# Kernel optimization log

Measured on AMD Instinct MI355X. Metric: run time of the kernel, lower is better.

## Reference

```python
import jax, jax.numpy as jnp
import numpy as np

B, T, F, U = 8192, 21, 3, 512


def setup_inputs() -> dict:
    key = jax.random.key(0)
    ks = jax.random.split(key, 10)
    s = 0.05  # weight scale
    return {
        "x": jax.random.normal(ks[0], (B, T, F), jnp.float32),
        "learn_type_all": jax.random.randint(ks[1], (T, B), 0, 2).astype(jnp.int32),
        "kernel": jax.random.normal(ks[2], (F, 4 * U), jnp.float32) * s,
        "recurrent_kernel": jax.random.normal(ks[3], (U, 4 * U), jnp.float32) * s,
        "bias": jnp.zeros((4 * U,), jnp.float32),
        "w_rnn": jax.random.normal(ks[4], (U, U), jnp.float32) * s,
        "u_rnn": jax.random.normal(ks[5], (U, U), jnp.float32) * s,
        "b_rnn": jnp.zeros((U,), jnp.float32),
        "w_fc": jax.random.normal(ks[6], (U, 32), jnp.float32) * s,
        "b_fc": jnp.zeros((32,), jnp.float32),
        "w_out": jax.random.normal(ks[7], (32, 1), jnp.float32) * s,
        "b_out": jnp.zeros((1,), jnp.float32),
    }


def _forward(x, learn_type_all, kernel, recurrent_kernel, bias,
             w_rnn, u_rnn, b_rnn, w_fc, b_fc, w_out, b_out):
    # Per-timestep, per-batch-row learn mask; if a timestep has no learned row,
    # the original forces row 0 to learn.
    mask = learn_type_all == 1                      # [T, B]
    any_learn = jnp.any(mask, axis=1)               # [T]
    mask = mask.at[:, 0].set(mask[:, 0] | ~any_learn)

    # For each row i, the output gate o comes from the most recent learned row
    # j <= i (forward fill); leading unlearned rows take the FIRST learned row's o.
    pos = jnp.where(mask, jnp.arange(B)[None, :], -1)      # [T, B]
    last_idx = jax.lax.cummax(pos, axis=1)                 # [T, B]
    first = jnp.argmax(mask, axis=1)                       # [T]
    o_idx = jnp.where(last_idx < 0, first[:, None], last_idx)  # [T, B]

    xs = jnp.moveaxis(x, 1, 0)  # [T, B, F]

    def lstm_cell(carry, inp):
        h, c = carry
        x_t, m_t, idx_t = inp
        # fused gate compute (implementation=2 path of the original)
        z = x_t @ kernel + h @ recurrent_kernel + bias     # [B, 4U]
        zi, zf, zg, zo = jnp.split(z, 4, axis=1)
        i_g = jax.nn.sigmoid(zi)
        f_g = jax.nn.sigmoid(zf)
        g_g = jnp.tanh(zg)
        o_comp = jax.nn.sigmoid(zo)
        # learned rows update carry; unlearned rows keep c_tm1
        c_new = jnp.where(m_t[:, None], f_g * c + i_g * g_g, c)
        o = o_comp[idx_t]                                  # gather prev-learned o
        h_new = o * jnp.tanh(c_new)
        return (h_new, c_new), h_new

    init = (jnp.zeros((B, U), x.dtype), jnp.zeros((B, U), x.dtype))
    (_, _), hs = jax.lax.scan(lstm_cell, init, (xs, mask, o_idx))  # hs: [T, B, U]

    # SimpleRNN over the LSTM output sequence (dropout inactive at inference)
    def srnn_cell(h, x_t):
        h_new = jnp.tanh(x_t @ w_rnn + h @ u_rnn + b_rnn)
        return h_new, None

    h_last, _ = jax.lax.scan(srnn_cell, jnp.zeros((B, U), x.dtype), hs)

    out = (h_last @ w_fc + b_fc) @ w_out + b_out           # [B, 1]
    return out


def reference(x, learn_type_all, kernel, recurrent_kernel, bias,
              w_rnn, u_rnn, b_rnn, w_fc, b_fc, w_out, b_out):
    return _forward(x, learn_type_all, kernel, recurrent_kernel, bias,
                    w_rnn, u_rnn, b_rnn, w_fc, b_fc, w_out, b_out)
```

## Files before the change

### kernel.cpp

```cpp
#include <hip/hip_runtime.h>
#include <stdint.h>

#define B_ 8192
#define T_ 21
#define F_ 3
#define U_ 512

typedef _Float16 f16x8 __attribute__((ext_vector_type(8)));
typedef float f32x4 __attribute__((ext_vector_type(4)));

__device__ __forceinline__ float fsigmoid(float x) { return 1.0f / (1.0f + __expf(-x)); }
__device__ __forceinline__ float ftanh_(float x) {
  float t = __expf(-2.0f * fabsf(x));
  float r = (1.0f - t) / (1.0f + t);
  return x < 0.0f ? -r : r;
}

__device__ __forceinline__ void gl_lds16(const void* g, void* l) {
  __builtin_amdgcn_global_load_lds((__attribute__((address_space(1))) void*)g,
                                   (__attribute__((address_space(3))) void*)l, 16, 0, 0);
}

__global__ void prep_weights(const float* __restrict__ Wr, const float* __restrict__ wrnn,
                             const float* __restrict__ urnn, const float* __restrict__ kern,
                             const float* __restrict__ bias,
                             _Float16* __restrict__ WrT, _Float16* __restrict__ W2T,
                             float* __restrict__ Kp, float* __restrict__ bp) {
  size_t i = (size_t)blockIdx.x * 256 + threadIdx.x;
  if (i < (size_t)2048 * 512) {
    int p = (int)(i >> 9), k = (int)(i & 511);
    int orig = ((p >> 4) & 3) * 512 + ((p >> 6) << 4) + (p & 15);
    WrT[i] = (_Float16)Wr[(size_t)k * 2048 + orig];
  }
  if (i < (size_t)512 * 1024) {
    int n = (int)(i >> 10), k = (int)(i & 1023);
    float v = (k < 512) ? wrnn[(size_t)k * 512 + n] : urnn[(size_t)(k - 512) * 512 + n];
    W2T[i] = (_Float16)v;
  }
  if (i < 2048) {
    int p = (int)i;
    int orig = ((p >> 4) & 3) * 512 + ((p >> 6) << 4) + (p & 15);
    Kp[p] = kern[orig];
    Kp[2048 + p] = kern[2048 + orig];
    Kp[4096 + p] = kern[4096 + orig];
    bp[p] = bias[orig];
  }
}

__global__ void prep_wv(const float* __restrict__ wfc, const float* __restrict__ bfc,
                        const float* __restrict__ wout, const float* __restrict__ bout,
                        float* __restrict__ wv) {
  int u = blockIdx.x * 256 + threadIdx.x;
  if (u < 512) {
    float s = 0.0f;
    for (int k = 0; k < 32; ++k) s += wfc[u * 32 + k] * wout[k];
    wv[u] = s;
  }
  if (u == 0) {
    float s = 0.0f;
    for (int k = 0; k < 32; ++k) s += bfc[k] * wout[k];
    wv[512] = s + bout[0];
  }
}

__global__ void prep_mask(const int* __restrict__ lt, int* __restrict__ orow,
                          int* __restrict__ idxL, int* __restrict__ Mpad) {
  const int t = blockIdx.x;
  const int tid = threadIdx.x;
  __shared__ int sh[1024];
  __shared__ int s_any, s_first;
  if (tid == 0) { s_any = 0; s_first = 0x7fffffff; }
  __syncthreads();
  const int base = tid * 8;
  const int* row = lt + (size_t)t * B_ + base;
  int bits = 0;
#pragma unroll
  for (int j = 0; j < 8; ++j) bits |= (row[j] == 1) << j;
  if (bits) atomicOr(&s_any, 1);
  __syncthreads();
  if (tid == 0 && !s_any) bits |= 1;
  if (bits) atomicMin(&s_first, base + __ffs(bits) - 1);
  int lmax = -1;
#pragma unroll
  for (int j = 0; j < 8; ++j)
    if ((bits >> j) & 1) lmax = base + j;
  sh[tid] = lmax;
  __syncthreads();
  for (int off = 1; off < 1024; off <<= 1) {
    int v = (tid >= off) ? sh[tid - off] : -1;
    __syncthreads();
    if (v > sh[tid]) sh[tid] = v;
    __syncthreads();
  }
  const int prefix = (tid > 0) ? sh[tid - 1] : -1;
  __syncthreads();
  const int cnt = __popc(bits);
  sh[tid] = cnt;
  __syncthreads();
  for (int off = 1; off < 1024; off <<= 1) {
    int v = (tid >= off) ? sh[tid - off] : 0;
    __syncthreads();
    sh[tid] += v;
    __syncthreads();
  }
  const int excl = sh[tid] - cnt;
  const int total = sh[1023];
  const int first = s_first;
  int run = prefix, pos = excl;
  int* orp = orow + (size_t)t * B_ + base;
  int* ixp = idxL + (size_t)t * B_;
#pragma unroll
  for (int j = 0; j < 8; ++j) {
    if ((bits >> j) & 1) { ixp[pos++] = base + j; run = base + j; }
    orp[j] = (run < 0) ? first : run;
  }
  const int padded = (total + 127) & ~127;
  if (tid < padded - total) ixp[total + tid] = -1;
  if (tid == 0) Mpad[t] = padded;
}

template <int MODE>
__device__ __forceinline__ void gemm_body(
    _Float16 (*__restrict__ Ab)[4096], _Float16 (*__restrict__ Bb)[4096],
    const _Float16* __restrict__ A0, const _Float16* __restrict__ A1,
    const _Float16* __restrict__ Wt, const float* __restrict__ x,
    const float* __restrict__ Kp, const float* __restrict__ bp,
    float* __restrict__ cbuf, _Float16* __restrict__ og,
    const float* __restrict__ brnn, _Float16* __restrict__ rout,
    const int* __restrict__ idxL, int mBase, int nBase, int t) {
  constexpr int K = (MODE == 0) ? 512 : 1024;
  constexpr int NT = K / 32;
  const int tid = threadIdx.x;
  const int w = tid >> 6, l = tid & 63;
  const int wm = w >> 1, wn = w & 1;
  const int lr = l >> 2;
  const int lk = (l & 3) * 8;
  const int ch0 = w * 2, ch1 = w * 2 + 1;

  int ra0, ra1;
  if constexpr (MODE == 0) {
    int i0 = idxL[mBase + ch0 * 16 + lr];
    int i1 = idxL[mBase + ch1 * 16 + lr];
    ra0 = i0 < 0 ? 0 : i0;
    ra1 = i1 < 0 ? 0 : i1;
  } else {
    ra0 = mBase + ch0 * 16 + lr;
    ra1 = mBase + ch1 * 16 + lr;
  }

  auto STAGE = [&](int bb, int kt) {
    const int k0 = kt * 32;
    const _Float16* As = A0;
    int koff = k0;
    if constexpr (MODE == 1) {
      if (k0 >= 512) { As = A1; koff = k0 - 512; }
    }
    gl_lds16(As + (size_t)ra0 * 512 + koff + lk, (char*)Ab[bb] + ch0 * 1024);
    gl_lds16(As + (size_t)ra1 * 512 + koff + lk, (char*)Ab[bb] + ch1 * 1024);
    gl_lds16(Wt + (size_t)(nBase + ch0 * 16 + lr) * K + k0 + lk, (char*)Bb[bb] + ch0 * 1024);
    gl_lds16(Wt + (size_t)(nBase + ch1 * 16 + lr) * K + k0 + lk, (char*)Bb[bb] + ch1 * 1024);
  };

  f32x4 acc[4][4] = {};
  STAGE(0, 0);
  const int frow = l & 15;
  const int fkb = (l >> 4) * 8;
  for (int kt = 0; kt < NT; ++kt) {
    __syncthreads();
    if (kt + 1 < NT) STAGE((kt + 1) & 1, kt + 1);
    const int bb = kt & 1;
    f16x8 af[4], bf[4];
#pragma unroll
    for (int m = 0; m < 4; ++m)
      af[m] = *(const f16x8*)&Ab[bb][(wm * 64 + m * 16 + frow) * 32 + fkb];
#pragma unroll
    for (int n = 0; n < 4; ++n)
      bf[n] = *(const f16x8*)&Bb[bb][(wn * 64 + n * 16 + frow) * 32 + fkb];
#pragma unroll
    for (int m = 0; m < 4; ++m)
#pragma unroll
      for (int n = 0; n < 4; ++n)
        acc[m][n] = __builtin_amdgcn_mfma_f32_16x16x32_f16(af[m], bf[n], acc[m][n], 0, 0, 0);
  }

  const int c_ = l & 15, rg = l >> 4;
  const int pB = nBase + wn * 64;
  if constexpr (MODE == 0) {
    const int u = (pB >> 6) * 16 + c_;
    float kf[4][3], bb4[4];
#pragma unroll
    for (int n = 0; n < 4; ++n) {
      int p = pB + n * 16 + c_;
      kf[n][0] = Kp[p]; kf[n][1] = Kp[2048 + p]; kf[n][2] = Kp[4096 + p];
      bb4[n] = bp[p];
    }
#pragma unroll
    for (int m = 0; m < 4; ++m) {
#pragma unroll
      for (int r = 0; r < 4; ++r) {
        int bi = idxL[mBase + wm * 64 + m * 16 + rg * 4 + r];
        if (bi < 0) continue;
        const float* xp = x + (size_t)bi * (T_ * F_) + t * F_;
        float x0 = xp[0], x1 = xp[1], x2 = xp[2];
        float zi = acc[m][0][r] + x0 * kf[0][0] + x1 * kf[0][1] + x2 * kf[0][2] + bb4[0];
        float zf = acc[m][1][r] + x0 * kf[1][0] + x1 * kf[1][1] + x2 * kf[1][2] + bb4[1];
        float zg = acc[m][2][r] + x0 * kf[2][0] + x1 * kf[2][1] + x2 * kf[2][2] + bb4[2];
        float zo = acc[m][3][r] + x0 * kf[3][0] + x1 * kf[3][1] + x2 * kf[3][2] + bb4[3];
        float ig = fsigmoid(zi), fg = fsigmoid(zf);
        float gg = ftanh_(zg), ogv = fsigmoid(zo);
        size_t ci = (size_t)bi * 512 + u;
        float cold = cbuf[ci];
        cbuf[ci] = fg * cold + ig * gg;
        og[ci] = (_Float16)ogv;
      }
    }
  } else {
#pragma unroll
    for (int m = 0; m < 4; ++m)
#pragma unroll
      for (int n = 0; n < 4; ++n) {
        int uu = pB + n * 16 + c_;
        float bn = brnn[uu];
#pragma unroll
        for (int r = 0; r < 4; ++r) {
          int b = mBase + wm * 64 + m * 16 + rg * 4 + r;
          rout[(size_t)b * 512 + uu] = (_Float16)ftanh_(acc[m][n][r] + bn);
        }
      }
  }
}

__global__ __launch_bounds__(256, 2) void fused_step(
    const _Float16* __restrict__ h, const _Float16* __restrict__ rin,
    _Float16* __restrict__ rot, const _Float16* __restrict__ WrT,
    const _Float16* __restrict__ W2T, const float* __restrict__ x,
    const float* __restrict__ Kp, const float* __restrict__ bp,
    float* __restrict__ cbuf, _Float16* __restrict__ og,
    const float* __restrict__ brnn, const int* __restrict__ idxL,
    const int* __restrict__ MpadP, int t) {
  __shared__ __align__(16) _Float16 Ab[2][4096];
  __shared__ __align__(16) _Float16 Bb[2][4096];
  if (blockIdx.y < 16) {
    if ((int)blockIdx.x * 128 >= *MpadP) return;
    gemm_body<0>(Ab, Bb, h, nullptr, WrT, x, Kp, bp, cbuf, og, nullptr, nullptr,
                 idxL, blockIdx.x * 128, blockIdx.y * 128, t);
  } else {
    gemm_body<1>(Ab, Bb, h, rin, W2T, nullptr, nullptr, nullptr, nullptr, nullptr,
                 brnn, rot, nullptr, blockIdx.x * 128, ((int)blockIdx.y - 16) * 128, t);
  }
}

__global__ __launch_bounds__(256, 2) void rnn_tail(
    const _Float16* __restrict__ h, const _Float16* __restrict__ rin,
    const _Float16* __restrict__ W2T, const float* __restrict__ brnn,
    _Float16* __restrict__ rot) {
  __shared__ __align__(16) _Float16 Ab[2][4096];
  __shared__ __align__(16) _Float16 Bb[2][4096];
  gemm_body<1>(Ab, Bb, h, rin, W2T, nullptr, nullptr, nullptr, nullptr, nullptr,
               brnn, rot, nullptr, blockIdx.x * 128, blockIdx.y * 128, 0);
}

__global__ void gather_h(const _Float16* __restrict__ og, const float* __restrict__ cbuf,
                         const int* __restrict__ orow, _Float16* __restrict__ h) {
  int g = blockIdx.x * 256 + threadIdx.x;
  int b = g >> 6, u0 = (g & 63) << 3;
  int src = orow[b];
  f16x8 ov = *(const f16x8*)(og + (size_t)src * 512 + u0);
  const float4* cp = (const float4*)(cbuf + (size_t)b * 512 + u0);
  float4 c0 = cp[0], c1 = cp[1];
  float cc[8] = {c0.x, c0.y, c0.z, c0.w, c1.x, c1.y, c1.z, c1.w};
  f16x8 hv;
#pragma unroll
  for (int j = 0; j < 8; ++j) hv[j] = (_Float16)((float)ov[j] * ftanh_(cc[j]));
  *(f16x8*)(h + (size_t)b * 512 + u0) = hv;
}

__global__ void final_fc(const _Float16* __restrict__ r, const float* __restrict__ wv,
                         float* __restrict__ out) {
  int gw = (blockIdx.x * 256 + threadIdx.x) >> 6;
  int l = threadIdx.x & 63;
  const _Float16* rr = r + (size_t)gw * 512;
  f16x8 rv = *(const f16x8*)(rr + l * 8);
  const float4* wp = (const float4*)(wv + l * 8);
  float4 w0 = wp[0], w1 = wp[1];
  float wf[8] = {w0.x, w0.y, w0.z, w0.w, w1.x, w1.y, w1.z, w1.w};
  float s = 0.0f;
#pragma unroll
  for (int j = 0; j < 8; ++j) s += (float)rv[j] * wf[j];
  for (int o = 32; o; o >>= 1) s += __shfl_down(s, o);
  if (l == 0) out[gw] = s + wv[512];
}

extern "C" void kernel_launch(void* const* d_in, const int* in_sizes, int n_in,
                              void* d_out, int out_size, void* d_ws, size_t ws_size,
                              hipStream_t stream) {
  const float* x    = (const float*)d_in[0];
  const int*   lt   = (const int*)d_in[1];
  const float* kern = (const float*)d_in[2];
  const float* Wr   = (const float*)d_in[3];
  const float* bias = (const float*)d_in[4];
  const float* wrnn = (const float*)d_in[5];
  const float* urnn = (const float*)d_in[6];
  const float* brnn = (const float*)d_in[7];
  const float* wfc  = (const float*)d_in[8];
  const float* bfc  = (const float*)d_in[9];
  const float* wout = (const float*)d_in[10];
  const float* bout = (const float*)d_in[11];

  char* ws = (char*)d_ws;
  size_t off = 0;
  auto alloc = [&](size_t bytes) {
    void* p = ws + off;
    off = (off + bytes + 255) & ~(size_t)255;
    return p;
  };
  int*      orow = (int*)alloc((size_t)T_ * B_ * 4);
  int*      idxL = (int*)alloc((size_t)T_ * B_ * 4);
  int*      Mpad = (int*)alloc(T_ * 4);
  float*    cbuf = (float*)alloc((size_t)B_ * U_ * 4);
  _Float16* h    = (_Float16*)alloc((size_t)B_ * U_ * 2);
  _Float16* r0   = (_Float16*)alloc((size_t)B_ * U_ * 2);
  _Float16* r1   = (_Float16*)alloc((size_t)B_ * U_ * 2);
  _Float16* og   = (_Float16*)alloc((size_t)B_ * U_ * 2);
  _Float16* WrT  = (_Float16*)alloc((size_t)2048 * 512 * 2);
  _Float16* W2T  = (_Float16*)alloc((size_t)512 * 1024 * 2);
  float*    Kp   = (float*)alloc(3 * 2048 * 4);
  float*    bp   = (float*)alloc(2048 * 4);
  float*    wv   = (float*)alloc(516 * 4);

  hipMemsetAsync(cbuf, 0, (size_t)B_ * U_ * 4, stream);
  hipMemsetAsync(h, 0, (size_t)B_ * U_ * 2, stream);
  hipMemsetAsync(r0, 0, (size_t)B_ * U_ * 2, stream);

  prep_weights<<<4096, 256, 0, stream>>>(Wr, wrnn, urnn, kern, bias, WrT, W2T, Kp, bp);
  prep_wv<<<2, 256, 0, stream>>>(wfc, bfc, wout, bout, wv);
  prep_mask<<<T_, 1024, 0, stream>>>(lt, orow, idxL, Mpad);

  _Float16* rin = r0;
  _Float16* rot = r1;
  fused_step<<<dim3(64, 16), 256, 0, stream>>>(h, nullptr, nullptr, WrT, W2T, x, Kp, bp,
                                               cbuf, og, brnn, idxL, Mpad, 0);
  gather_h<<<2048, 256, 0, stream>>>(og, cbuf, orow, h);
  for (int t = 1; t < T_; ++t) {
    fused_step<<<dim3(64, 20), 256, 0, stream>>>(h, rin, rot, WrT, W2T, x, Kp, bp,
                                                 cbuf, og, brnn,
                                                 idxL + (size_t)t * B_, Mpad + t, t);
    _Float16* tmp = rin; rin = rot; rot = tmp;
    gather_h<<<2048, 256, 0, stream>>>(og, cbuf, orow + (size_t)t * B_, h);
  }
  rnn_tail<<<dim3(64, 4), 256, 0, stream>>>(h, rin, W2T, brnn, rot);
  final_fc<<<2048, 256, 0, stream>>>(rot, wv, (float*)d_out);
}
```

Before: 1.025 ms.

## Triple-buffer GEMM LDS pipeline and compute learned-row h in epilogue

The GEMM main loop moves from a double-buffered LDS stage with one barrier per step to a three-stage ring. It prefetches two K-tiles ahead and uses explicit vmcnt waits and raw barriers, with launch bounds raised to 3 blocks per CU. The LSTM epilogue now writes h directly for learned rows into a double-buffered h array. prep_mask builds an index list of unlearned rows so gather_h only processes those rows. This aims to hide global-load latency and cut gather work, at the cost of more LDS per block, an extra h buffer, and fragile hand-tuned waitcnt counts.

```diff
diff --git a/kernel.cpp b/kernel.cpp
--- a/kernel.cpp
+++ b/kernel.cpp
@@ -64,7 +64,8 @@
 }
 
 __global__ void prep_mask(const int* __restrict__ lt, int* __restrict__ orow,
-                          int* __restrict__ idxL, int* __restrict__ Mpad) {
+                          int* __restrict__ idxL, int* __restrict__ idxU,
+                          int* __restrict__ Mpad) {
   const int t = blockIdx.x;
   const int tid = threadIdx.x;
   __shared__ int sh[1024];
@@ -106,16 +107,20 @@
   const int excl = sh[tid] - cnt;
   const int total = sh[1023];
   const int first = s_first;
-  int run = prefix, pos = excl;
+  int run = prefix, posL = excl, posU = base - excl;
   int* orp = orow + (size_t)t * B_ + base;
-  int* ixp = idxL + (size_t)t * B_;
+  int* ixL = idxL + (size_t)t * B_;
+  int* ixU = idxU + (size_t)t * B_;
 #pragma unroll
   for (int j = 0; j < 8; ++j) {
-    if ((bits >> j) & 1) { ixp[pos++] = base + j; run = base + j; }
+    if ((bits >> j) & 1) { ixL[posL++] = base + j; run = base + j; }
+    else                 { ixU[posU++] = base + j; }
     orp[j] = (run < 0) ? first : run;
   }
   const int padded = (total + 127) & ~127;
-  if (tid < padded - total) ixp[total + tid] = -1;
+  if (tid < padded - total) ixL[total + tid] = -1;
+  const int totU = B_ - total;
+  for (int i = totU + tid; i < B_; i += 1024) ixU[i] = -1;
   if (tid == 0) Mpad[t] = padded;
 }
 
@@ -126,8 +131,9 @@
     const _Float16* __restrict__ Wt, const float* __restrict__ x,
     const float* __restrict__ Kp, const float* __restrict__ bp,
     float* __restrict__ cbuf, _Float16* __restrict__ og,
-    const float* __restrict__ brnn, _Float16* __restrict__ rout,
-    const int* __restrict__ idxL, int mBase, int nBase, int t) {
+    _Float16* __restrict__ hnew, const float* __restrict__ brnn,
+    _Float16* __restrict__ rout, const int* __restrict__ idxL,
+    int mBase, int nBase, int t) {
   constexpr int K = (MODE == 0) ? 512 : 1024;
   constexpr int NT = K / 32;
   const int tid = threadIdx.x;
@@ -163,12 +169,22 @@
 
   f32x4 acc[4][4] = {};
   STAGE(0, 0);
+  STAGE(1, 1);
   const int frow = l & 15;
   const int fkb = (l >> 4) * 8;
+#pragma unroll
   for (int kt = 0; kt < NT; ++kt) {
-    __syncthreads();
-    if (kt + 1 < NT) STAGE((kt + 1) & 1, kt + 1);
-    const int bb = kt & 1;
+    if (kt + 2 < NT) {
+      STAGE((kt + 2) % 3, kt + 2);
+      asm volatile("s_waitcnt vmcnt(8)" ::: "memory");
+    } else if (kt + 1 < NT) {
+      asm volatile("s_waitcnt vmcnt(4)" ::: "memory");
+    } else {
+      asm volatile("s_waitcnt vmcnt(0)" ::: "memory");
+    }
+    __builtin_amdgcn_s_barrier();
+    __builtin_amdgcn_sched_barrier(0);
+    const int bb = kt % 3;
     f16x8 af[4], bf[4];
 #pragma unroll
     for (int m = 0; m < 4; ++m)
@@ -181,6 +197,8 @@
 #pragma unroll
       for (int n = 0; n < 4; ++n)
         acc[m][n] = __builtin_amdgcn_mfma_f32_16x16x32_f16(af[m], bf[n], acc[m][n], 0, 0, 0);
+    __builtin_amdgcn_sched_barrier(0);
+    __builtin_amdgcn_s_barrier();
   }
 
   const int c_ = l & 15, rg = l >> 4;
@@ -210,8 +228,10 @@
         float gg = ftanh_(zg), ogv = fsigmoid(zo);
         size_t ci = (size_t)bi * 512 + u;
         float cold = cbuf[ci];
-        cbuf[ci] = fg * cold + ig * gg;
+        float cnew = fg * cold + ig * gg;
+        cbuf[ci] = cnew;
         og[ci] = (_Float16)ogv;
+        hnew[ci] = (_Float16)(ogv * ftanh_(cnew));
       }
     }
   } else {
@@ -230,40 +250,43 @@
   }
 }
 
-__global__ __launch_bounds__(256, 2) void fused_step(
-    const _Float16* __restrict__ h, const _Float16* __restrict__ rin,
-    _Float16* __restrict__ rot, const _Float16* __restrict__ WrT,
-    const _Float16* __restrict__ W2T, const float* __restrict__ x,
-    const float* __restrict__ Kp, const float* __restrict__ bp,
-    float* __restrict__ cbuf, _Float16* __restrict__ og,
-    const float* __restrict__ brnn, const int* __restrict__ idxL,
-    const int* __restrict__ MpadP, int t) {
-  __shared__ __align__(16) _Float16 Ab[2][4096];
-  __shared__ __align__(16) _Float16 Bb[2][4096];
+__global__ __launch_bounds__(256, 3) void fused_step(
+    const _Float16* __restrict__ hprev, _Float16* __restrict__ hnew,
+    const _Float16* __restrict__ rin, _Float16* __restrict__ rot,
+    const _Float16* __restrict__ WrT, const _Float16* __restrict__ W2T,
+    const float* __restrict__ x, const float* __restrict__ Kp,
+    const float* __restrict__ bp, float* __restrict__ cbuf,
+    _Float16* __restrict__ og, const float* __restrict__ brnn,
+    const int* __restrict__ idxL, const int* __restrict__ MpadP, int t) {
+  __shared__ __align__(16) _Float16 Ab[3][4096];
+  __shared__ __align__(16) _Float16 Bb[3][4096];
   if (blockIdx.y < 16) {
     if ((int)blockIdx.x * 128 >= *MpadP) return;
-    gemm_body<0>(Ab, Bb, h, nullptr, WrT, x, Kp, bp, cbuf, og, nullptr, nullptr,
-                 idxL, blockIdx.x * 128, blockIdx.y * 128, t);
+    gemm_body<0>(Ab, Bb, hprev, nullptr, WrT, x, Kp, bp, cbuf, og, hnew, nullptr,
+                 nullptr, idxL, blockIdx.x * 128, blockIdx.y * 128, t);
   } else {
-    gemm_body<1>(Ab, Bb, h, rin, W2T, nullptr, nullptr, nullptr, nullptr, nullptr,
-                 brnn, rot, nullptr, blockIdx.x * 128, ((int)blockIdx.y - 16) * 128, t);
-  }
-}
-
-__global__ __launch_bounds__(256, 2) void rnn_tail(
+    gemm_body<1>(Ab, Bb, hprev, rin, W2T, nullptr, nullptr, nullptr, nullptr, nullptr,
+                 nullptr, brnn, rot, nullptr, blockIdx.x * 128, ((int)blockIdx.y - 16) * 128, t);
+  }
+}
+
+__global__ __launch_bounds__(256, 3) void rnn_tail(
     const _Float16* __restrict__ h, const _Float16* __restrict__ rin,
     const _Float16* __restrict__ W2T, const float* __restrict__ brnn,
     _Float16* __restrict__ rot) {
-  __shared__ __align__(16) _Float16 Ab[2][4096];
-  __shared__ __align__(16) _Float16 Bb[2][4096];
+  __shared__ __align__(16) _Float16 Ab[3][4096];
+  __shared__ __align__(16) _Float16 Bb[3][4096];
   gemm_body<1>(Ab, Bb, h, rin, W2T, nullptr, nullptr, nullptr, nullptr, nullptr,
-               brnn, rot, nullptr, blockIdx.x * 128, blockIdx.y * 128, 0);
+               nullptr, brnn, rot, nullptr, blockIdx.x * 128, blockIdx.y * 128, 0);
 }
 
 __global__ void gather_h(const _Float16* __restrict__ og, const float* __restrict__ cbuf,
-                         const int* __restrict__ orow, _Float16* __restrict__ h) {
+                         const int* __restrict__ orow, const int* __restrict__ idxU,
+                         _Float16* __restrict__ h) {
   int g = blockIdx.x * 256 + threadIdx.x;
-  int b = g >> 6, u0 = (g & 63) << 3;
+  int b = idxU[g >> 6];
+  if (b < 0) return;
+  int u0 = (g & 63) << 3;
   int src = orow[b];
   f16x8 ov = *(const f16x8*)(og + (size_t)src * 512 + u0);
   const float4* cp = (const float4*)(cbuf + (size_t)b * 512 + u0);
@@ -316,9 +339,11 @@
   };
   int*      orow = (int*)alloc((size_t)T_ * B_ * 4);
   int*      idxL = (int*)alloc((size_t)T_ * B_ * 4);
+  int*      idxU = (int*)alloc((size_t)T_ * B_ * 4);
   int*      Mpad = (int*)alloc(T_ * 4);
   float*    cbuf = (float*)alloc((size_t)B_ * U_ * 4);
-  _Float16* h    = (_Float16*)alloc((size_t)B_ * U_ * 2);
+  _Float16* h0   = (_Float16*)alloc((size_t)B_ * U_ * 2);
+  _Float16* h1   = (_Float16*)alloc((size_t)B_ * U_ * 2);
   _Float16* r0   = (_Float16*)alloc((size_t)B_ * U_ * 2);
   _Float16* r1   = (_Float16*)alloc((size_t)B_ * U_ * 2);
   _Float16* og   = (_Float16*)alloc((size_t)B_ * U_ * 2);
@@ -329,25 +354,29 @@
   float*    wv   = (float*)alloc(516 * 4);
 
   hipMemsetAsync(cbuf, 0, (size_t)B_ * U_ * 4, stream);
-  hipMemsetAsync(h, 0, (size_t)B_ * U_ * 2, stream);
+  hipMemsetAsync(h0, 0, (size_t)B_ * U_ * 2, stream);
   hipMemsetAsync(r0, 0, (size_t)B_ * U_ * 2, stream);
 
   prep_weights<<<4096, 256, 0, stream>>>(Wr, wrnn, urnn, kern, bias, WrT, W2T, Kp, bp);
   prep_wv<<<2, 256, 0, stream>>>(wfc, bfc, wout, bout, wv);
-  prep_mask<<<T_, 1024, 0, stream>>>(lt, orow, idxL, Mpad);
-
+  prep_mask<<<T_, 1024, 0, stream>>>(lt, orow, idxL, idxU, Mpad);
+
+  _Float16* hbuf[2] = {h0, h1};
   _Float16* rin = r0;
   _Float16* rot = r1;
-  fused_step<<<dim3(64, 16), 256, 0, stream>>>(h, nullptr, nullptr, WrT, W2T, x, Kp, bp,
-                                               cbuf, og, brnn, idxL, Mpad, 0);
-  gather_h<<<2048, 256, 0, stream>>>(og, cbuf, orow, h);
+  fused_step<<<dim3(64, 16), 256, 0, stream>>>(h0, h1, nullptr, nullptr, WrT, W2T, x,
+                                               Kp, bp, cbuf, og, brnn, idxL, Mpad, 0);
+  gather_h<<<2048, 256, 0, stream>>>(og, cbuf, orow, idxU, h1);
   for (int t = 1; t < T_; ++t) {
-    fused_step<<<dim3(64, 20), 256, 0, stream>>>(h, rin, rot, WrT, W2T, x, Kp, bp,
+    _Float16* hp = hbuf[t & 1];
+    _Float16* hn = hbuf[(t + 1) & 1];
+    fused_step<<<dim3(64, 20), 256, 0, stream>>>(hp, hn, rin, rot, WrT, W2T, x, Kp, bp,
                                                  cbuf, og, brnn,
                                                  idxL + (size_t)t * B_, Mpad + t, t);
     _Float16* tmp = rin; rin = rot; rot = tmp;
-    gather_h<<<2048, 256, 0, stream>>>(og, cbuf, orow + (size_t)t * B_, h);
-  }
-  rnn_tail<<<dim3(64, 4), 256, 0, stream>>>(h, rin, W2T, brnn, rot);
+    gather_h<<<2048, 256, 0, stream>>>(og, cbuf, orow + (size_t)t * B_,
+                                       idxU + (size_t)t * B_, hn);
+  }
+  rnn_tail<<<dim3(64, 4), 256, 0, stream>>>(hbuf[T_ & 1], rin, W2T, brnn, rot);
   final_fc<<<2048, 256, 0, stream>>>(rot, wv, (float*)d_out);
 }
```

Result: faster. 975.6 us (-4.8%).
